# Kernel tuning notes

Measured on AMD Instinct MI355X. Metric: run time of the kernel, lower is better.

## Reference

```python
import jax, jax.numpy as jnp
import numpy as np

B, V, H, W = 8, 2, 1024, 1024
N = 131072
TH_MIN, TH_MAX = 0.0, 500.0
ALPHA = 0.5


def _make_extrinsics():
    # Random small-rotation camera-to-world poses (invertible 4x4), fixed seed.
    rng = np.random.default_rng(0)
    E = np.tile(np.eye(4, dtype=np.float32), (B, V, 1, 1))
    for bi in range(B):
        for vi in range(V):
            ang = rng.uniform(-0.15, 0.15)
            ax = rng.normal(size=3)
            ax = ax / np.linalg.norm(ax)
            K = np.array([[0.0, -ax[2], ax[1]], [ax[2], 0.0, -ax[0]], [-ax[1], ax[0], 0.0]])
            R = np.eye(3) + np.sin(ang) * K + (1.0 - np.cos(ang)) * (K @ K)
            E[bi, vi, :3, :3] = R.astype(np.float32)
            E[bi, vi, :3, 3] = (rng.normal(size=3) * 0.5).astype(np.float32)
    return jnp.asarray(E)


def setup_inputs():
    key = jax.random.key(0)
    k0, k1, k2, k3, k4 = jax.random.split(key, 5)
    scale = jnp.array([W - 1.0, H - 1.0], jnp.float32)
    mkpts0 = jax.random.uniform(k0, (N, 2), dtype=jnp.float32) * scale
    mkpts1 = jax.random.uniform(k1, (N, 2), dtype=jnp.float32) * scale
    mconf = jax.random.uniform(k2, (N,), jnp.float32, 0.2, 1.0)
    mbids = jnp.sort(jax.random.randint(k3, (N,), 0, B, dtype=jnp.int32))
    intr = jnp.tile(jnp.array([[1.0, 0.0, 0.5], [0.0, 1.0, 0.5], [0.0, 0.0, 1.0]], jnp.float32), (B, V, 1, 1))
    extr = _make_extrinsics()
    disps = jax.random.uniform(k4, (V * B, 1, H, W), jnp.float32, 0.01, 1.0)
    return {"mkpts0": mkpts0, "mkpts1": mkpts1, "mconf": mconf, "mbids": mbids,
            "intrinsics": intr, "extrinsics": extr, "fullres_disps": disps}


def _forward(mkpts0, mkpts1, mconf, mbids, intrinsics, extrinsics, fullres_disps):
    b, v = intrinsics.shape[:2]
    _, _, h, w = fullres_disps.shape
    # intr0[0,:]*=w ; intr0[1,:]*=h  (normalized -> pixel intrinsics)
    row_scale = jnp.array([float(w), float(h), 1.0], intrinsics.dtype)[None, None, :, None]
    intr = intrinsics * row_scale                                    # (b,v,3,3)
    extr_inv = jnp.linalg.inv(extrinsics)                            # (b,v,4,4)
    proj = jnp.einsum('bvij,bvjk->bvik', intr, extr_inv[:, :, :3, :])  # (b,v,3,4)

    # --- per-keypoint DLT triangulation (vectorized over all N matches) ---
    P = proj[mbids]                                                  # (N,v,3,4)
    pts2 = jnp.stack([mkpts0, mkpts1], axis=1)                       # (N,v,2)
    # rows: conf*(x*P[2]-P[0]), conf*(y*P[2]-P[1])
    A = P[:, :, 2:3, :] * pts2[..., None] - P[:, :, :2, :]           # (N,v,2,4)
    A = A * mconf[:, None, None, None]
    A = A.reshape(-1, 2 * v, 4)                                      # (N,4,4)
    _, _, vh = jnp.linalg.svd(A, full_matrices=False)
    hom = vh[:, -1, :]                                               # last right singular vector
    pts_world = hom[:, :3] / hom[:, 3:4]                             # (N,3)

    # transform into each camera frame: pc_transform(pts, extr.inverse())
    pw_h = jnp.concatenate([pts_world, jnp.ones_like(pts_world[:, :1])], axis=-1)
    pts_cam = jnp.einsum('nvij,nj->nvi', extr_inv[mbids], pw_h)[..., :3]  # (N,v,3)
    z = pts_cam[..., 2]                                              # (N,v)
    valid = jnp.all((z > TH_MIN) & (z < TH_MAX), axis=1)             # (N,)

    # --- near/far over valid matched depths per (scene, view) ---
    zmin = jnp.where(valid[:, None], z, jnp.inf)
    zmax = jnp.where(valid[:, None], z, -jnp.inf)
    near = jax.ops.segment_min(zmin, mbids, num_segments=b)          # (b,v)
    far = jax.ops.segment_max(zmax, mbids, num_segments=b)
    has = jax.ops.segment_max(valid.astype(jnp.float32), mbids, num_segments=b)
    flag = jnp.broadcast_to(has[:, None], (b, v))                    # (b,v)
    near = jnp.where(flag > 0, near, 0.0)
    far = jnp.where(flag > 0, far, 500.0)

    # --- fusion_mkpt_costvolum: scatter 1/z into the cost-volume disparities ---
    disps = fullres_disps.reshape(v, b, h, w)                        # '(v b) 1 h w'
    mk_x = jnp.clip(jnp.stack([mkpts0[:, 0], mkpts1[:, 0]], 1).astype(jnp.int32), 0, w - 1)  # (N,v)
    mk_y = jnp.clip(jnp.stack([mkpts0[:, 1], mkpts1[:, 1]], 1).astype(jnp.int32), 0, h - 1)
    mk_z = 1.0 / z                                                   # matched disparity (N,v)
    view_idx = jnp.broadcast_to(jnp.arange(v, dtype=jnp.int32)[None, :], mk_x.shape)
    bids2 = jnp.broadcast_to(mbids[:, None], mk_x.shape)
    cost = disps[view_idx, bids2, mk_y, mk_x]                        # gather existing disparity
    val = ALPHA * mk_z + (1.0 - ALPHA) * cost                        # alpha-weighted fusion
    val = jnp.where(valid[:, None], val, cost)                       # masked-out matches: no-op write
    disps = disps.at[view_idx, bids2, mk_y, mk_x].set(val)
    fused = disps.reshape(v * b, 1, h, w)
    return fused, near, far, flag


def reference(mkpts0, mkpts1, mconf, mbids, intrinsics, extrinsics, fullres_disps):
    return _forward(mkpts0, mkpts1, mconf, mbids, intrinsics, extrinsics, fullres_disps)
```

## Files before the change

### kernel.cpp

```cpp
#include <hip/hip_runtime.h>
#include <math.h>

#define BB 8
#define VV 2
#define HH 1024
#define WW 1024
#define NPTS 131072
#define IMG (HH*WW)
#define FUSED (VV*BB*IMG)

#define NSOLVE (NPTS/256)
#define NCOPY  (FUSED/4/256)

typedef float f32x4 __attribute__((ext_vector_type(4)));

#define OFF_VAL  0u
#define OFF_PIX  (8u*NPTS)
#define OFF_RED  (16u*NPTS)
#define OFF_WIN  (OFF_RED + 0x20000u)
#define WS_NEED  ((size_t)OFF_WIN + 4ull*(size_t)FUSED)

__device__ __forceinline__ int clampi(int v, int lo, int hi) {
    return v < lo ? lo : (v > hi ? hi : v);
}

__device__ __forceinline__ void prep_one(int t, const float* __restrict__ intr,
                                         const float* __restrict__ extr, double* sD) {
    const float* E = extr + t * 16;
    double R[3][3], tr[3];
#pragma unroll
    for (int i = 0; i < 3; i++) {
#pragma unroll
        for (int j = 0; j < 3; j++) R[i][j] = (double)E[i * 4 + j];
        tr[i] = (double)E[i * 4 + 3];
    }
    double inv[3][4];
#pragma unroll
    for (int i = 0; i < 3; i++) {
#pragma unroll
        for (int j = 0; j < 3; j++) inv[i][j] = R[j][i];
        inv[i][3] = -(R[0][i] * tr[0] + R[1][i] * tr[1] + R[2][i] * tr[2]);
    }
    const float* K = intr + t * 9;
    double rs[3] = {(double)WW, (double)HH, 1.0};
#pragma unroll
    for (int i = 0; i < 3; i++)
#pragma unroll
        for (int k = 0; k < 4; k++) {
            double s = 0.0;
#pragma unroll
            for (int j = 0; j < 3; j++) s += (double)K[i * 3 + j] * rs[i] * inv[j][k];
            sD[t * 12 + i * 4 + k] = s;
        }
#pragma unroll
    for (int k = 0; k < 4; k++) sD[192 + t * 4 + k] = inv[2][k];
}

template <int DEDUP>
__global__ __launch_bounds__(256) void mega_kernel(
        const f32x4* __restrict__ src, f32x4* __restrict__ dst,
        const float2* __restrict__ mk0, const float2* __restrict__ mk1,
        const int* __restrict__ mbids,
        const float* __restrict__ intr, const float* __restrict__ extr,
        const float* __restrict__ disps,
        float* __restrict__ out, char* __restrict__ ws) {
    int b = blockIdx.x, t = threadIdx.x;

    if (b >= NSOLVE) {
        int i = (b - NSOLVE) * 256 + t;
        f32x4 v = src[i];
        __builtin_nontemporal_store(v, &dst[i]);
        return;
    }

    __shared__ double sD[256];
    __shared__ int nearB[16], farB[16], hasB[8];
    if (t < 16) {
        prep_one(t, intr, extr, sD);
        nearB[t] = 0x7F800000;
        farB[t]  = 0;
        if (t < 8) hasB[t] = 0;
    }
    __syncthreads();

    int n = b * 256 + t;
    float* valarr = (float*)(ws + OFF_VAL);
    int*   pixarr = (int*)(ws + OFF_PIX);
    int*   winner = (int*)(ws + OFF_WIN);

    int bid = mbids[n];
    float2 q0 = mk0[n], q1 = mk1[n];
    float xf[2] = {q0.x, q1.x};
    float yf[2] = {q0.y, q1.y};

    double M[4][4];
#pragma unroll
    for (int i = 0; i < 4; i++)
#pragma unroll
        for (int j = 0; j < 4; j++) M[i][j] = 0.0;
#pragma unroll
    for (int v = 0; v < 2; v++) {
        const double* P = sD + (bid * VV + v) * 12;
        double xx = (double)xf[v], yy = (double)yf[v];
        double r0[4], r1[4];
#pragma unroll
        for (int j = 0; j < 4; j++) {
            r0[j] = xx * P[8 + j] - P[j];
            r1[j] = yy * P[8 + j] - P[4 + j];
        }
#pragma unroll
        for (int i = 0; i < 4; i++)
#pragma unroll
            for (int j = 0; j < 4; j++) M[i][j] += r0[i] * r0[j] + r1[i] * r1[j];
    }

    double Vm[4][4] = {{1, 0, 0, 0}, {0, 1, 0, 0}, {0, 0, 1, 0}, {0, 0, 0, 1}};
    for (int sweep = 0; sweep < 8; ++sweep) {
        double off = fabs(M[0][1]) + fabs(M[0][2]) + fabs(M[0][3]) +
                     fabs(M[1][2]) + fabs(M[1][3]) + fabs(M[2][3]);
        double dia = fabs(M[0][0]) + fabs(M[1][1]) + fabs(M[2][2]) + fabs(M[3][3]);
        if (off <= 1e-13 * dia) break;
#pragma unroll
        for (int p = 0; p < 3; p++) {
#pragma unroll
            for (int q = p + 1; q < 4; q++) {
                double apq = M[p][q];
                if (fabs(apq) < 1e-300) continue;
                double tau = (M[q][q] - M[p][p]) / (2.0 * apq);
                double rt  = sqrt(1.0 + tau * tau);
                double t_  = (tau >= 0.0) ? 1.0 / (tau + rt) : 1.0 / (tau - rt);
                double c = 1.0 / sqrt(1.0 + t_ * t_);
                double s = t_ * c;
#pragma unroll
                for (int k = 0; k < 4; k++) {
                    double mp = M[k][p], mq = M[k][q];
                    M[k][p] = c * mp - s * mq;
                    M[k][q] = s * mp + c * mq;
                }
#pragma unroll
                for (int k = 0; k < 4; k++) {
                    double mp = M[p][k], mq = M[q][k];
                    M[p][k] = c * mp - s * mq;
                    M[q][k] = s * mp + c * mq;
                }
#pragma unroll
                for (int k = 0; k < 4; k++) {
                    double vp = Vm[k][p], vq = Vm[k][q];
                    Vm[k][p] = c * vp - s * vq;
                    Vm[k][q] = s * vp + c * vq;
                }
            }
        }
    }
    int jmin = 0; double dmin = M[0][0];
    if (M[1][1] < dmin) { dmin = M[1][1]; jmin = 1; }
    if (M[2][2] < dmin) { dmin = M[2][2]; jmin = 2; }
    if (M[3][3] < dmin) { dmin = M[3][3]; jmin = 3; }

    double ev[4];
#pragma unroll
    for (int i = 0; i < 4; i++) {
        double a01 = (jmin == 0) ? Vm[i][0] : Vm[i][1];
        double a23 = (jmin == 2) ? Vm[i][2] : Vm[i][3];
        ev[i] = (jmin < 2) ? a01 : a23;
    }
    double iw  = 1.0 / ev[3];
    double pwx = ev[0] * iw, pwy = ev[1] * iw, pwz = ev[2] * iw;

    double z[2];
#pragma unroll
    for (int v = 0; v < 2; v++) {
        const double* e = sD + 192 + (bid * VV + v) * 4;
        z[v] = e[0] * pwx + e[1] * pwy + e[2] * pwz + e[3];
    }
    bool valid = (z[0] > 0.0) && (z[0] < 500.0) && (z[1] > 0.0) && (z[1] < 500.0);

    unsigned long long vb = __ballot(valid);
    int bidFirst = __shfl(bid, 0);
    int bidLast  = __shfl(bid, 63);
    if (bidFirst == bidLast) {
        if (vb != 0ULL) {
            float zn[2], zf[2];
#pragma unroll
            for (int v = 0; v < 2; v++) {
                zn[v] = valid ? (float)z[v] : INFINITY;
                zf[v] = valid ? (float)z[v] : -1.0f;
            }
#pragma unroll
            for (int off = 32; off > 0; off >>= 1) {
#pragma unroll
                for (int v = 0; v < 2; v++) {
                    zn[v] = fminf(zn[v], __shfl_down(zn[v], off));
                    zf[v] = fmaxf(zf[v], __shfl_down(zf[v], off));
                }
            }
            if ((t & 63) == 0) {
#pragma unroll
                for (int v = 0; v < 2; v++) {
                    atomicMin(&nearB[bid * VV + v], __float_as_int(zn[v]));
                    atomicMax(&farB[bid * VV + v],  __float_as_int(zf[v]));
                }
                atomicOr(&hasB[bid], 1);
            }
        }
    } else if (valid) {
#pragma unroll
        for (int v = 0; v < 2; v++) {
            int fb = __float_as_int((float)z[v]);
            atomicMin(&nearB[bid * VV + v], fb);
            atomicMax(&farB[bid * VV + v],  fb);
        }
        atomicOr(&hasB[bid], 1);
    }

#pragma unroll
    for (int v = 0; v < 2; v++) {
        int xi = clampi((int)xf[v], 0, WW - 1);
        int yi = clampi((int)yf[v], 0, HH - 1);
        int pix = (v * BB + bid) * IMG + yi * WW + xi;
        float cost = disps[pix];
        if (DEDUP) {
            winner[pix] = 0;
            valarr[2 * n + v] = valid ? (float)(0.5 * (1.0 / z[v]) + 0.5 * (double)cost)
                                      : 0.0f;
            pixarr[2 * n + v] = pix;
        } else {
            float val = valid ? (float)(0.5 * (1.0 / z[v]) + 0.5 * (double)cost) : cost;
            out[pix] = val;
        }
    }

    __syncthreads();
    int* red = (int*)(ws + OFF_RED) + b * 40;
    if (t < 16) {
        red[t]      = nearB[t];
        red[16 + t] = farB[t];
        if (t < 8) red[32 + t] = hasB[t];
    }
}

__device__ __forceinline__ void reduce_nearfar(const char* __restrict__ ws,
                                               float* __restrict__ out) {
    __shared__ int redLds[40];
    int t = threadIdx.x;
    const int* red = (const int*)(ws + OFF_RED);
    int w = t >> 6, lane = t & 63;
    for (int c = w; c < 40; c += 4) {
        int acc = (c < 16) ? 0x7F800000 : 0;
        for (int s = lane; s < NSOLVE; s += 64) {
            int vv = red[s * 40 + c];
            acc = (c < 16) ? min(acc, vv) : (c < 32 ? max(acc, vv) : (acc | vv));
        }
#pragma unroll
        for (int off = 32; off > 0; off >>= 1) {
            int o = __shfl_down(acc, off);
            acc = (c < 16) ? min(acc, o) : (c < 32 ? max(acc, o) : (acc | o));
        }
        if (lane == 0) redLds[c] = acc;
    }
    __syncthreads();
    if (t < 16) {
        int hv = redLds[32 + (t >> 1)];
        out[FUSED + t]               = hv ? __int_as_float(redLds[t])      : 0.0f;
        out[FUSED + BB * VV + t]     = hv ? __int_as_float(redLds[16 + t]) : 500.0f;
        out[FUSED + 2 * BB * VV + t] = hv ? 1.0f : 0.0f;
    }
}

__global__ __launch_bounds__(256) void vote_kernel(char* __restrict__ ws,
                                                   float* __restrict__ out) {
    int gid = blockIdx.x * 256 + threadIdx.x;
    const int2* pix2 = (const int2*)(ws + OFF_PIX);
    int* winner = (int*)(ws + OFF_WIN);
    int2 p = pix2[gid];
    atomicMax(winner + p.x, 2 * gid + 1);
    atomicMax(winner + p.y, 2 * gid + 2);
    if (blockIdx.x == 0) reduce_nearfar(ws, out);
}

__global__ __launch_bounds__(256) void resolve_kernel(float* __restrict__ out,
                                                      const char* __restrict__ ws) {
    int gid = blockIdx.x * 256 + threadIdx.x;
    const int2*   pix2 = (const int2*)(ws + OFF_PIX);
    const float2* val2 = (const float2*)(ws + OFF_VAL);
    const int*    winner = (const int*)(ws + OFF_WIN);
    int2 p = pix2[gid];
    float2 v = val2[gid];
    if (v.x > 0.0f && winner[p.x] == 2 * gid + 1) out[p.x] = v.x;
    if (v.y > 0.0f && winner[p.y] == 2 * gid + 2) out[p.y] = v.y;
}

__global__ __launch_bounds__(256) void reduce_kernel(float* __restrict__ out,
                                                     const char* __restrict__ ws) {
    reduce_nearfar(ws, out);
}

extern "C" void kernel_launch(void* const* d_in, const int* in_sizes, int n_in,
                              void* d_out, int out_size, void* d_ws, size_t ws_size,
                              hipStream_t stream) {
    const float* mk0   = (const float*)d_in[0];
    const float* mk1   = (const float*)d_in[1];
    const int*   mbids = (const int*)d_in[3];
    const float* intr  = (const float*)d_in[4];
    const float* extr  = (const float*)d_in[5];
    const float* disps = (const float*)d_in[6];
    float* out = (float*)d_out;
    char*  ws  = (char*)d_ws;

    bool dedup = (ws_size >= WS_NEED);
    dim3 grid(NSOLVE + NCOPY);

    if (dedup) {
        mega_kernel<1><<<grid, 256, 0, stream>>>(
            (const f32x4*)disps, (f32x4*)out, (const float2*)mk0, (const float2*)mk1,
            mbids, intr, extr, disps, out, ws);
        vote_kernel<<<NSOLVE, 256, 0, stream>>>(ws, out);
        resolve_kernel<<<NSOLVE, 256, 0, stream>>>(out, ws);
    } else {
        mega_kernel<0><<<grid, 256, 0, stream>>>(
            (const f32x4*)disps, (f32x4*)out, (const float2*)mk0, (const float2*)mk1,
            mbids, intr, extr, disps, out, ws);
        reduce_kernel<<<1, 256, 0, stream>>>(out, ws);
    }
}
```

Before: 184.0 us.

## Split the disparity copy across solve and vote kernels to overlap the atomic voting

The bulk copy of the disparity volume into the output is now split in half. One half runs inside the solve kernel and the other half runs inside the vote kernel, so the copy overlaps with the atomic voting and the near/far reduction. Each copy block now moves four vec4 chunks, which cuts the block count. The risk is correctness ordering: the copy in the vote kernel must finish before resolve writes the winning pixels, and since resolve is a later launch on the same stream this holds. Load balance between the two halves may not be ideal.

After: 186.7 us. About the same (+1.5%).

```diff
diff --git a/kernel.cpp b/kernel.cpp
--- a/kernel.cpp
+++ b/kernel.cpp
@@ -10,7 +10,14 @@
 #define FUSED (VV*BB*IMG)
 
 #define NSOLVE (NPTS/256)
-#define NCOPY  (FUSED/4/256)
+#define F4TOT  (FUSED/4)
+
+#define PER_CP   4
+#define NC_K1    2048
+#define COPY_K1  (NC_K1*256*PER_CP)
+#define NC_K2    2048
+
+#define NC_FB    (F4TOT/(256*PER_CP))
 
 typedef float f32x4 __attribute__((ext_vector_type(4)));
 
@@ -54,6 +61,18 @@
         }
 #pragma unroll
     for (int k = 0; k < 4; k++) sD[192 + t * 4 + k] = inv[2][k];
+}
+
+__device__ __forceinline__ void copy_chunk(const f32x4* __restrict__ src,
+                                           f32x4* __restrict__ dst,
+                                           int base, int blk, int t) {
+    int s = base + blk * (256 * PER_CP);
+#pragma unroll
+    for (int k = 0; k < PER_CP; k++) {
+        int i = s + k * 256 + t;
+        f32x4 v = src[i];
+        __builtin_nontemporal_store(v, &dst[i]);
+    }
 }
 
 template <int DEDUP>
@@ -67,9 +86,7 @@
     int b = blockIdx.x, t = threadIdx.x;
 
     if (b >= NSOLVE) {
-        int i = (b - NSOLVE) * 256 + t;
-        f32x4 v = src[i];
-        __builtin_nontemporal_store(v, &dst[i]);
+        copy_chunk(src, dst, 0, b - NSOLVE, t);
         return;
     }
 
@@ -267,15 +284,21 @@
     }
 }
 
-__global__ __launch_bounds__(256) void vote_kernel(char* __restrict__ ws,
-                                                   float* __restrict__ out) {
-    int gid = blockIdx.x * 256 + threadIdx.x;
-    const int2* pix2 = (const int2*)(ws + OFF_PIX);
-    int* winner = (int*)(ws + OFF_WIN);
-    int2 p = pix2[gid];
-    atomicMax(winner + p.x, 2 * gid + 1);
-    atomicMax(winner + p.y, 2 * gid + 2);
-    if (blockIdx.x == 0) reduce_nearfar(ws, out);
+__global__ __launch_bounds__(256) void vote_copy_kernel(
+        const f32x4* __restrict__ src, f32x4* __restrict__ dst,
+        char* __restrict__ ws, float* __restrict__ out) {
+    int b = blockIdx.x, t = threadIdx.x;
+    copy_chunk(src, dst, COPY_K1, b, t);
+    if (b < NSOLVE) {
+        int gid = b * 256 + t;
+        const int2* pix2 = (const int2*)(ws + OFF_PIX);
+        int* winner = (int*)(ws + OFF_WIN);
+        int2 p = pix2[gid];
+        atomicMax(winner + p.x, 2 * gid + 1);
+        atomicMax(winner + p.y, 2 * gid + 2);
+    } else if (b == NSOLVE) {
+        reduce_nearfar(ws, out);
+    }
 }
 
 __global__ __launch_bounds__(256) void resolve_kernel(float* __restrict__ out,
@@ -308,16 +331,16 @@
     char*  ws  = (char*)d_ws;
 
     bool dedup = (ws_size >= WS_NEED);
-    dim3 grid(NSOLVE + NCOPY);
 
     if (dedup) {
-        mega_kernel<1><<<grid, 256, 0, stream>>>(
+        mega_kernel<1><<<dim3(NSOLVE + NC_K1), 256, 0, stream>>>(
             (const f32x4*)disps, (f32x4*)out, (const float2*)mk0, (const float2*)mk1,
             mbids, intr, extr, disps, out, ws);
-        vote_kernel<<<NSOLVE, 256, 0, stream>>>(ws, out);
+        vote_copy_kernel<<<NC_K2, 256, 0, stream>>>(
+            (const f32x4*)disps, (f32x4*)out, ws, out);
         resolve_kernel<<<NSOLVE, 256, 0, stream>>>(out, ws);
     } else {
-        mega_kernel<0><<<grid, 256, 0, stream>>>(
+        mega_kernel<0><<<dim3(NSOLVE + NC_FB), 256, 0, stream>>>(
             (const f32x4*)disps, (f32x4*)out, (const float2*)mk0, (const float2*)mk1,
             mbids, intr, extr, disps, out, ws);
         reduce_kernel<<<1, 256, 0, stream>>>(out, ws);
```
